# Performance work log

Hardware: AMD Instinct MI355X
Metric: run time of the kernel (lower is better)

The kernel has to match this reference:

```python
import jax, jax.numpy as jnp
import numpy as np
import math

NUM_HEADS = 2


def setup_inputs() -> dict:
    key = jax.random.key(0)
    k1, k2, k3, k4 = jax.random.split(key, 4)
    B, S, E = 16, 2048, 8  # embed_dim == n_wires == 8 (required by module structure)
    x = jax.random.normal(k1, (B, S, E), dtype=jnp.float32)
    theta = jax.random.normal(k2, (E,), dtype=jnp.float32)          # trainable RX angles, one per wire
    w_out = jax.random.normal(k3, (E, E), dtype=jnp.float32) / math.sqrt(E)  # out_proj weight
    b_out = jax.random.normal(k4, (E,), dtype=jnp.float32) * 0.01   # out_proj bias
    return {"x": x, "theta": theta, "w_out": w_out, "b_out": b_out}


def reference(x, theta, w_out, b_out):
    B, S, E = x.shape
    H = NUM_HEADS
    dk = E // H
    # Quantum projection, analytic form: per-wire RX(x) then RX(theta) on |0>,
    # PauliZ expectation -> cos(x + theta). Same layer applied for q, k, v.
    q = jnp.cos(x + theta)              # [B, S, E]
    qh = q.reshape(B, S, H, dk).transpose(0, 2, 1, 3)  # [B, H, S, dk]; q == k == v
    scores = jnp.einsum('bhqd,bhkd->bhqk', qh, qh) / jnp.sqrt(jnp.float32(dk))
    attn = jax.nn.softmax(scores, axis=-1)             # dropout is identity in eval
    out = jnp.einsum('bhqk,bhkd->bhqd', attn, qh)      # [B, H, S, dk]
    out = out.transpose(0, 2, 1, 3).reshape(B, S, E)
    return out @ w_out.T + b_out
```

## Files before the change

kernel.cpp:

```cpp
#include <hip/hip_runtime.h>
#include <math.h>

#define BB 16
#define SS 2048
#define NF 330
#define NS 495
#define SPAD 512
#define NTILE 31

struct E4 { unsigned char e0, e1, e2, e3; };

struct Tables {
  E4 se[496];
  E4 fe[330];
  float fc[330];
  short sidx[330][5];
};

constexpr int T1c(int n){ return n+1; }
constexpr int T2c(int n){ return (n+1)*(n+2)/2; }
constexpr int T3c(int n){ return (n+1)*(n+2)*(n+3)/6; }
constexpr int rank8(int a,int b,int c,int d){
  int r = 0;
  for (int e0=0;e0<a;++e0) r += T3c(8-e0);
  for (int e1=0;e1<b;++e1) r += T2c(8-a-e1);
  for (int e2=0;e2<c;++e2) r += T1c(8-a-b-e2);
  return r + d;
}
constexpr double besselI2(int n){
  double t = 1.0;
  for (int i=1;i<=n;++i) t /= (double)i;
  double s = 0.0;
  for (int m=0;m<14;++m){ if (m>0) t /= (double)(m*(m+n)); s += t; }
  return s;
}
constexpr Tables gen(){
  Tables T{};
  double cheb[8] = {};
  for (int n=0;n<8;++n) cheb[n] = (n==0?1.0:2.0)*besselI2(n);
  const int tm[8][8] = {
    {1,0,0,0,0,0,0,0},{0,1,0,0,0,0,0,0},{-1,0,2,0,0,0,0,0},{0,-3,0,4,0,0,0,0},
    {1,0,-8,0,8,0,0,0},{0,5,0,-20,0,16,0,0},{-1,0,18,0,-48,0,32,0},{0,-7,0,56,0,-112,0,64}};
  double bk[8] = {};
  double p2 = 1.0;
  for (int k=0;k<8;++k){
    double tc = 0.0;
    for (int n=0;n<8;++n) tc += cheb[n]*(double)tm[n][k];
    bk[k] = tc/p2;
    p2 *= 2.0;
  }
  const double fact[9] = {1,1,2,6,24,120,720,5040,40320};
  {
    int idx = 0;
    for (int a=0;a<=8;++a) for (int b=0;b<=8-a;++b) for (int c=0;c<=8-a-b;++c)
      for (int d=0;d<=8-a-b-c;++d){
        T.se[idx].e0=(unsigned char)a; T.se[idx].e1=(unsigned char)b;
        T.se[idx].e2=(unsigned char)c; T.se[idx].e3=(unsigned char)d; ++idx;
      }
  }
  {
    int idx = 0;
    for (int a=0;a<=7;++a) for (int b=0;b<=7-a;++b) for (int c=0;c<=7-a-b;++c)
      for (int d=0;d<=7-a-b-c;++d){
        const int k = a+b+c+d;
        const double mult = fact[k]/(fact[a]*fact[b]*fact[c]*fact[d]);
        double pk = 1.0; for (int i=0;i<k;++i) pk *= 2.0;
        T.fe[idx].e0=(unsigned char)a; T.fe[idx].e1=(unsigned char)b;
        T.fe[idx].e2=(unsigned char)c; T.fe[idx].e3=(unsigned char)d;
        T.fc[idx] = (float)(bk[k]*mult/pk);
        T.sidx[idx][0] = (short)rank8(a+1,b,c,d);
        T.sidx[idx][1] = (short)rank8(a,b+1,c,d);
        T.sidx[idx][2] = (short)rank8(a,b,c+1,d);
        T.sidx[idx][3] = (short)rank8(a,b,c,d+1);
        T.sidx[idx][4] = (short)rank8(a,b,c,d);
        ++idx;
      }
  }
  return T;
}
constexpr Tables TAB = gen();

template<int T>
__device__ __forceinline__ void sum_tile(const float4* __restrict__ x4,
                                         float4 th, int b, int h, int t,
                                         float* __restrict__ wsbh){
  float acc[16];
#pragma unroll
  for (int i=0;i<16;++i) acc[i] = 0.f;
  for (int rr=0; rr<8; ++rr){
    const int s = (rr<<8) + t;
    float4 xr = x4[(size_t)(b*SS+s)*2 + h];
    const float q0 = __cosf(xr.x + th.x), q1 = __cosf(xr.y + th.y),
                q2 = __cosf(xr.z + th.z), q3 = __cosf(xr.w + th.w);
    float p0[9], p1[9], p2[9], p3[9];
    p0[0]=1.f; p1[0]=1.f; p2[0]=1.f; p3[0]=1.f;
#pragma unroll
    for (int e=1;e<9;++e){
      p0[e]=p0[e-1]*q0; p1[e]=p1[e-1]*q1; p2[e]=p2[e-1]*q2; p3[e]=p3[e-1]*q3;
    }
#pragma unroll
    for (int i=0;i<16;++i){
      if (T*16+i < NS){
        const E4 e = TAB.se[T*16+i];
        acc[i] += p0[e.e0]*p1[e.e1]*p2[e.e2]*p3[e.e3];
      }
    }
  }
  const int lane = (int)(threadIdx.x & 63);
#pragma unroll
  for (int i=0;i<16;++i){
    if (T*16+i < NS){
      float v = acc[i];
#pragma unroll
      for (int st=1; st<64; st<<=1) v += __shfl_xor(v, st, 64);
      if (lane == 0) atomicAdd(wsbh + T*16 + i, v);
    }
  }
}

__global__ __launch_bounds__(256)
void qsum_kernel(const float* __restrict__ x, const float* __restrict__ theta,
                 float* __restrict__ ws){
  const int tile = blockIdx.x & 31;
  if (tile >= NTILE) return;
  const int bh = blockIdx.x >> 5;
  const int b = bh >> 1, h = bh & 1;
  const int t = (int)threadIdx.x;
  const float4 th = ((const float4*)theta)[h];
  const float4* x4 = (const float4*)x;
  float* wsbh = ws + (size_t)bh * SPAD;
  switch(tile){
#define KCASE(n) case n: sum_tile<n>(x4, th, b, h, t, wsbh); break;
    KCASE(0) KCASE(1) KCASE(2) KCASE(3) KCASE(4) KCASE(5) KCASE(6) KCASE(7)
    KCASE(8) KCASE(9) KCASE(10) KCASE(11) KCASE(12) KCASE(13) KCASE(14) KCASE(15)
    KCASE(16) KCASE(17) KCASE(18) KCASE(19) KCASE(20) KCASE(21) KCASE(22) KCASE(23)
    KCASE(24) KCASE(25) KCASE(26) KCASE(27) KCASE(28) KCASE(29) KCASE(30)
#undef KCASE
  }
}

__global__ __launch_bounds__(256)
void qout_kernel(const float* __restrict__ x, const float* __restrict__ theta,
                 const float* __restrict__ ws, const float* __restrict__ w_out,
                 const float* __restrict__ b_out, float* __restrict__ out){
  __shared__ float po[128 * 8];
  const int t   = (int)threadIdx.x;
  const int blk = (int)blockIdx.x;
  const int b   = blk >> 4;
  const int s0  = (blk & 15) << 7;
  const int lane = t & 63;
  const int h  = __builtin_amdgcn_readfirstlane((t >> 6) & 1);
  const int rr = ((t >> 7) << 6) | lane;
  const int s  = s0 + rr;

  const float4 th = ((const float4*)theta)[h];
  float4 xr = ((const float4*)x)[(size_t)(b*SS+s)*2 + h];
  const float q0 = __cosf(xr.x + th.x), q1 = __cosf(xr.y + th.y),
              q2 = __cosf(xr.z + th.z), q3 = __cosf(xr.w + th.w);
  float p0[8], p1[8], p2[8], p3[8];
  p0[0]=1.f; p1[0]=1.f; p2[0]=1.f; p3[0]=1.f;
#pragma unroll
  for (int e=1;e<8;++e){
    p0[e]=p0[e-1]*q0; p1[e]=p1[e-1]*q1; p2[e]=p2[e-1]*q2; p3[e]=p3[e-1]*q3;
  }
  const float* Sp = ws + (size_t)((b<<1) + h) * SPAD;
  float n0=0.f, n1=0.f, n2=0.f, n3=0.f, dn=0.f;
#pragma unroll
  for (int F=0; F<NF; ++F){
    const E4 e = TAB.fe[F];
    const float m = p0[e.e0]*p1[e.e1]*p2[e.e2]*p3[e.e3]*TAB.fc[F];
    n0 = fmaf(m, Sp[TAB.sidx[F][0]], n0);
    n1 = fmaf(m, Sp[TAB.sidx[F][1]], n1);
    n2 = fmaf(m, Sp[TAB.sidx[F][2]], n2);
    n3 = fmaf(m, Sp[TAB.sidx[F][3]], n3);
    dn = fmaf(m, Sp[TAB.sidx[F][4]], dn);
  }
  const float inv = 1.0f / dn;
  po[rr*8 + h*4 + 0] = n0*inv;
  po[rr*8 + h*4 + 1] = n1*inv;
  po[rr*8 + h*4 + 2] = n2*inv;
  po[rr*8 + h*4 + 3] = n3*inv;
  __syncthreads();

  if (t < 128){
    const float* pr = po + t*8;
    float o[8];
#pragma unroll
    for (int j=0;j<8;++j) o[j] = pr[j];
    float r[8];
#pragma unroll
    for (int e=0;e<8;++e){
      float acc = b_out[e];
#pragma unroll
      for (int j=0;j<8;++j) acc = fmaf(o[j], w_out[e*8+j], acc);
      r[e] = acc;
    }
    float* op = out + ((size_t)(b*SS + s0 + t)) * 8;
    *(float4*)op       = make_float4(r[0], r[1], r[2], r[3]);
    *(float4*)(op + 4) = make_float4(r[4], r[5], r[6], r[7]);
  }
}

extern "C" void kernel_launch(void* const* d_in, const int* in_sizes, int n_in,
                              void* d_out, int out_size, void* d_ws, size_t ws_size,
                              hipStream_t stream) {
  const float* x     = (const float*)d_in[0];
  const float* theta = (const float*)d_in[1];
  const float* w_out = (const float*)d_in[2];
  const float* b_out = (const float*)d_in[3];
  float* out = (float*)d_out;
  (void)in_sizes; (void)n_in; (void)out_size; (void)ws_size;

  (void)hipMemsetAsync(d_ws, 0, (size_t)32 * SPAD * sizeof(float), stream);
  qsum_kernel<<<dim3(32 * 32), 256, 0, stream>>>(x, theta, (float*)d_ws);
  qout_kernel<<<dim3(BB * 16), 256, 0, stream>>>(x, theta, (const float*)d_ws,
                                                 w_out, b_out, out);
}
```

Measured before the change: 88.90 us.

## Lower exp polynomial degree to 6 and pregather scaled moment coefficients

New measurement: 83.38 us. 6.2% less time.

```diff
diff --git a/kernel.cpp b/kernel.cpp
--- a/kernel.cpp
+++ b/kernel.cpp
@@ -1,148 +1,195 @@
 #include <hip/hip_runtime.h>
+#include <utility>
 #include <math.h>
 
 #define BB 16
 #define SS 2048
-#define NF 330
-#define NS 495
-#define SPAD 512
-#define NTILE 31
-
-struct E4 { unsigned char e0, e1, e2, e3; };
-
-struct Tables {
-  E4 se[496];
-  E4 fe[330];
-  float fc[330];
-  short sidx[330][5];
-};
-
-constexpr int T1c(int n){ return n+1; }
-constexpr int T2c(int n){ return (n+1)*(n+2)/2; }
-constexpr int T3c(int n){ return (n+1)*(n+2)*(n+3)/6; }
-constexpr int rank8(int a,int b,int c,int d){
+#define NF 210
+#define NS 330
+#define SSTR 336
+#define GSTR 224
+#define GBH (5*GSTR)
+#define GBASE 16384
+#define NTILE 21
+
+struct E4 { int e0, e1, e2, e3; };
+
+constexpr E4 exp_at(int idx, int deg) {
   int r = 0;
-  for (int e0=0;e0<a;++e0) r += T3c(8-e0);
-  for (int e1=0;e1<b;++e1) r += T2c(8-a-e1);
-  for (int e2=0;e2<c;++e2) r += T1c(8-a-b-e2);
-  return r + d;
-}
-constexpr double besselI2(int n){
+  for (int a = 0; a <= deg; ++a)
+    for (int b = 0; b <= deg - a; ++b)
+      for (int c = 0; c <= deg - a - b; ++c)
+        for (int d = 0; d <= deg - a - b - c; ++d) {
+          if (r == idx) return E4{a, b, c, d};
+          ++r;
+        }
+  return E4{0, 0, 0, 0};
+}
+constexpr int rank_of(int a, int b, int c, int d, int deg) {
+  int r = 0;
+  for (int aa = 0; aa <= deg; ++aa)
+    for (int bb = 0; bb <= deg - aa; ++bb)
+      for (int cc = 0; cc <= deg - aa - bb; ++cc)
+        for (int dd = 0; dd <= deg - aa - bb - cc; ++dd) {
+          if (aa == a && bb == b && cc == c && dd == d) return r;
+          ++r;
+        }
+  return 0;
+}
+constexpr double besselI2(int n) {
   double t = 1.0;
-  for (int i=1;i<=n;++i) t /= (double)i;
+  for (int i = 1; i <= n; ++i) t /= (double)i;
   double s = 0.0;
-  for (int m=0;m<14;++m){ if (m>0) t /= (double)(m*(m+n)); s += t; }
+  for (int m = 0; m < 16; ++m) { if (m > 0) t /= (double)(m * (m + n)); s += t; }
   return s;
 }
-constexpr Tables gen(){
-  Tables T{};
-  double cheb[8] = {};
-  for (int n=0;n<8;++n) cheb[n] = (n==0?1.0:2.0)*besselI2(n);
-  const int tm[8][8] = {
-    {1,0,0,0,0,0,0,0},{0,1,0,0,0,0,0,0},{-1,0,2,0,0,0,0,0},{0,-3,0,4,0,0,0,0},
-    {1,0,-8,0,8,0,0,0},{0,5,0,-20,0,16,0,0},{-1,0,18,0,-48,0,32,0},{0,-7,0,56,0,-112,0,64}};
-  double bk[8] = {};
+
+struct FTab { int sidx[NF][5]; float fc[NF]; };
+constexpr FTab gen_ftab() {
+  FTab T{};
+  double cheb[7] = {};
+  for (int n = 0; n < 7; ++n) cheb[n] = (n == 0 ? 1.0 : 2.0) * besselI2(n);
+  const int tm[7][7] = {
+    {1,0,0,0,0,0,0},{0,1,0,0,0,0,0},{-1,0,2,0,0,0,0},{0,-3,0,4,0,0,0},
+    {1,0,-8,0,8,0,0},{0,5,0,-20,0,16,0},{-1,0,18,0,-48,0,32}};
+  double bk[7] = {};
   double p2 = 1.0;
-  for (int k=0;k<8;++k){
+  for (int k = 0; k < 7; ++k) {
     double tc = 0.0;
-    for (int n=0;n<8;++n) tc += cheb[n]*(double)tm[n][k];
-    bk[k] = tc/p2;
+    for (int n = 0; n < 7; ++n) tc += cheb[n] * (double)tm[n][k];
+    bk[k] = tc / p2;
     p2 *= 2.0;
   }
-  const double fact[9] = {1,1,2,6,24,120,720,5040,40320};
-  {
-    int idx = 0;
-    for (int a=0;a<=8;++a) for (int b=0;b<=8-a;++b) for (int c=0;c<=8-a-b;++c)
-      for (int d=0;d<=8-a-b-c;++d){
-        T.se[idx].e0=(unsigned char)a; T.se[idx].e1=(unsigned char)b;
-        T.se[idx].e2=(unsigned char)c; T.se[idx].e3=(unsigned char)d; ++idx;
-      }
-  }
-  {
-    int idx = 0;
-    for (int a=0;a<=7;++a) for (int b=0;b<=7-a;++b) for (int c=0;c<=7-a-b;++c)
-      for (int d=0;d<=7-a-b-c;++d){
-        const int k = a+b+c+d;
-        const double mult = fact[k]/(fact[a]*fact[b]*fact[c]*fact[d]);
-        double pk = 1.0; for (int i=0;i<k;++i) pk *= 2.0;
-        T.fe[idx].e0=(unsigned char)a; T.fe[idx].e1=(unsigned char)b;
-        T.fe[idx].e2=(unsigned char)c; T.fe[idx].e3=(unsigned char)d;
-        T.fc[idx] = (float)(bk[k]*mult/pk);
-        T.sidx[idx][0] = (short)rank8(a+1,b,c,d);
-        T.sidx[idx][1] = (short)rank8(a,b+1,c,d);
-        T.sidx[idx][2] = (short)rank8(a,b,c+1,d);
-        T.sidx[idx][3] = (short)rank8(a,b,c,d+1);
-        T.sidx[idx][4] = (short)rank8(a,b,c,d);
-        ++idx;
-      }
-  }
+  const double fact[8] = {1,1,2,6,24,120,720,5040};
+  int idx = 0;
+  for (int a = 0; a <= 6; ++a)
+    for (int b = 0; b <= 6 - a; ++b)
+      for (int c = 0; c <= 6 - a - b; ++c)
+        for (int d = 0; d <= 6 - a - b - c; ++d) {
+          const int k = a + b + c + d;
+          const double mult = fact[k] / (fact[a]*fact[b]*fact[c]*fact[d]);
+          double pk = 1.0; for (int i = 0; i < k; ++i) pk *= 2.0;
+          T.fc[idx] = (float)(bk[k] * mult / pk);
+          T.sidx[idx][0] = rank_of(a+1, b, c, d, 7);
+          T.sidx[idx][1] = rank_of(a, b+1, c, d, 7);
+          T.sidx[idx][2] = rank_of(a, b, c+1, d, 7);
+          T.sidx[idx][3] = rank_of(a, b, c, d+1, 7);
+          T.sidx[idx][4] = rank_of(a, b, c, d, 7);
+          ++idx;
+        }
   return T;
 }
-constexpr Tables TAB = gen();
-
+__constant__ constexpr FTab FT = gen_ftab();
+
+template<int IDX, int SLOT>
+__device__ __forceinline__ void acc_one(float* acc, const float* p0, const float* p1,
+                                        const float* p2, const float* p3) {
+  if constexpr (IDX < NS) {
+    constexpr E4 e = exp_at(IDX, 7);
+    acc[SLOT] += p0[e.e0] * p1[e.e1] * p2[e.e2] * p3[e.e3];
+  }
+}
+template<int T, int... I>
+__device__ __forceinline__ void acc_tile(float* acc, const float* p0, const float* p1,
+                                         const float* p2, const float* p3,
+                                         std::integer_sequence<int, I...>) {
+  (acc_one<T * 16 + I, I>(acc, p0, p1, p2, p3), ...);
+}
+template<int IDX, int SLOT>
+__device__ __forceinline__ void red_one(float* acc, int lane, float* wsbh) {
+  if constexpr (IDX < NS) {
+    float v = acc[SLOT];
+    v += __shfl_xor(v, 1, 64);  v += __shfl_xor(v, 2, 64);
+    v += __shfl_xor(v, 4, 64);  v += __shfl_xor(v, 8, 64);
+    v += __shfl_xor(v, 16, 64); v += __shfl_xor(v, 32, 64);
+    if (lane == 0) atomicAdd(wsbh + IDX, v);
+  }
+}
+template<int T, int... I>
+__device__ __forceinline__ void red_tile(float* acc, int lane, float* wsbh,
+                                         std::integer_sequence<int, I...>) {
+  (red_one<T * 16 + I, I>(acc, lane, wsbh), ...);
+}
 template<int T>
-__device__ __forceinline__ void sum_tile(const float4* __restrict__ x4,
-                                         float4 th, int b, int h, int t,
-                                         float* __restrict__ wsbh){
+__device__ __forceinline__ void sum_tile(const float4* x4, float4 th, int b, int h,
+                                         int t, float* wsbh) {
   float acc[16];
 #pragma unroll
-  for (int i=0;i<16;++i) acc[i] = 0.f;
-  for (int rr=0; rr<8; ++rr){
-    const int s = (rr<<8) + t;
-    float4 xr = x4[(size_t)(b*SS+s)*2 + h];
+  for (int i = 0; i < 16; ++i) acc[i] = 0.f;
+  for (int rr = 0; rr < 8; ++rr) {
+    const int s = (rr << 8) + t;
+    float4 xr = x4[(size_t)(b * SS + s) * 2 + h];
     const float q0 = __cosf(xr.x + th.x), q1 = __cosf(xr.y + th.y),
                 q2 = __cosf(xr.z + th.z), q3 = __cosf(xr.w + th.w);
-    float p0[9], p1[9], p2[9], p3[9];
-    p0[0]=1.f; p1[0]=1.f; p2[0]=1.f; p3[0]=1.f;
-#pragma unroll
-    for (int e=1;e<9;++e){
-      p0[e]=p0[e-1]*q0; p1[e]=p1[e-1]*q1; p2[e]=p2[e-1]*q2; p3[e]=p3[e-1]*q3;
+    float p0[8], p1[8], p2[8], p3[8];
+    p0[0] = 1.f; p1[0] = 1.f; p2[0] = 1.f; p3[0] = 1.f;
+#pragma unroll
+    for (int e = 1; e < 8; ++e) {
+      p0[e] = p0[e-1] * q0; p1[e] = p1[e-1] * q1;
+      p2[e] = p2[e-1] * q2; p3[e] = p3[e-1] * q3;
     }
-#pragma unroll
-    for (int i=0;i<16;++i){
-      if (T*16+i < NS){
-        const E4 e = TAB.se[T*16+i];
-        acc[i] += p0[e.e0]*p1[e.e1]*p2[e.e2]*p3[e.e3];
-      }
-    }
-  }
-  const int lane = (int)(threadIdx.x & 63);
-#pragma unroll
-  for (int i=0;i<16;++i){
-    if (T*16+i < NS){
-      float v = acc[i];
-#pragma unroll
-      for (int st=1; st<64; st<<=1) v += __shfl_xor(v, st, 64);
-      if (lane == 0) atomicAdd(wsbh + T*16 + i, v);
-    }
-  }
+    acc_tile<T>(acc, p0, p1, p2, p3, std::make_integer_sequence<int, 16>{});
+  }
+  red_tile<T>(acc, (int)(threadIdx.x & 63), wsbh, std::make_integer_sequence<int, 16>{});
 }
 
 __global__ __launch_bounds__(256)
 void qsum_kernel(const float* __restrict__ x, const float* __restrict__ theta,
-                 float* __restrict__ ws){
-  const int tile = blockIdx.x & 31;
-  if (tile >= NTILE) return;
-  const int bh = blockIdx.x >> 5;
+                 float* __restrict__ ws) {
+  const int tile = (int)blockIdx.x;
+  const int bh   = (int)blockIdx.y;
   const int b = bh >> 1, h = bh & 1;
   const int t = (int)threadIdx.x;
   const float4 th = ((const float4*)theta)[h];
   const float4* x4 = (const float4*)x;
-  float* wsbh = ws + (size_t)bh * SPAD;
-  switch(tile){
-#define KCASE(n) case n: sum_tile<n>(x4, th, b, h, t, wsbh); break;
-    KCASE(0) KCASE(1) KCASE(2) KCASE(3) KCASE(4) KCASE(5) KCASE(6) KCASE(7)
-    KCASE(8) KCASE(9) KCASE(10) KCASE(11) KCASE(12) KCASE(13) KCASE(14) KCASE(15)
-    KCASE(16) KCASE(17) KCASE(18) KCASE(19) KCASE(20) KCASE(21) KCASE(22) KCASE(23)
-    KCASE(24) KCASE(25) KCASE(26) KCASE(27) KCASE(28) KCASE(29) KCASE(30)
-#undef KCASE
-  }
+  float* wsbh = ws + (size_t)bh * SSTR;
+  switch (tile) {
+#define KC(n) case n: sum_tile<n>(x4, th, b, h, t, wsbh); break;
+    KC(0) KC(1) KC(2) KC(3) KC(4) KC(5) KC(6) KC(7) KC(8) KC(9) KC(10)
+    KC(11) KC(12) KC(13) KC(14) KC(15) KC(16) KC(17) KC(18) KC(19) KC(20)
+#undef KC
+  }
+}
+
+__global__ __launch_bounds__(256)
+void qg_kernel(const float* __restrict__ ws, float* __restrict__ wsg) {
+  const int bh = (int)blockIdx.x;
+  const int F  = (int)threadIdx.x;
+  if (F >= NF) return;
+  const float* Sp = ws + (size_t)bh * SSTR;
+  float* Gp = wsg + (size_t)bh * GBH;
+  const float c = FT.fc[F];
+  Gp[0 * GSTR + F] = c * Sp[FT.sidx[F][0]];
+  Gp[1 * GSTR + F] = c * Sp[FT.sidx[F][1]];
+  Gp[2 * GSTR + F] = c * Sp[FT.sidx[F][2]];
+  Gp[3 * GSTR + F] = c * Sp[FT.sidx[F][3]];
+  Gp[4 * GSTR + F] = c * Sp[FT.sidx[F][4]];
+}
+
+template<int F>
+__device__ __forceinline__ void feat_one(float* n, const float* __restrict__ Gp,
+                                         const float* p0, const float* p1,
+                                         const float* p2, const float* p3) {
+  constexpr E4 e = exp_at(F, 6);
+  const float m = p0[e.e0] * p1[e.e1] * p2[e.e2] * p3[e.e3];
+  n[0] = fmaf(m, Gp[0 * GSTR + F], n[0]);
+  n[1] = fmaf(m, Gp[1 * GSTR + F], n[1]);
+  n[2] = fmaf(m, Gp[2 * GSTR + F], n[2]);
+  n[3] = fmaf(m, Gp[3 * GSTR + F], n[3]);
+  n[4] = fmaf(m, Gp[4 * GSTR + F], n[4]);
+}
+template<int... F>
+__device__ __forceinline__ void feat_all(float* n, const float* __restrict__ Gp,
+                                         const float* p0, const float* p1,
+                                         const float* p2, const float* p3,
+                                         std::integer_sequence<int, F...>) {
+  (feat_one<F>(n, Gp, p0, p1, p2, p3), ...);
 }
 
 __global__ __launch_bounds__(256)
 void qout_kernel(const float* __restrict__ x, const float* __restrict__ theta,
-                 const float* __restrict__ ws, const float* __restrict__ w_out,
-                 const float* __restrict__ b_out, float* __restrict__ out){
+                 const float* __restrict__ wsg, const float* __restrict__ w_out,
+                 const float* __restrict__ b_out, float* __restrict__ out) {
   __shared__ float po[128 * 8];
   const int t   = (int)threadIdx.x;
   const int blk = (int)blockIdx.x;
@@ -154,48 +201,41 @@
   const int s  = s0 + rr;
 
   const float4 th = ((const float4*)theta)[h];
-  float4 xr = ((const float4*)x)[(size_t)(b*SS+s)*2 + h];
+  float4 xr = ((const float4*)x)[(size_t)(b * SS + s) * 2 + h];
   const float q0 = __cosf(xr.x + th.x), q1 = __cosf(xr.y + th.y),
               q2 = __cosf(xr.z + th.z), q3 = __cosf(xr.w + th.w);
-  float p0[8], p1[8], p2[8], p3[8];
-  p0[0]=1.f; p1[0]=1.f; p2[0]=1.f; p3[0]=1.f;
-#pragma unroll
-  for (int e=1;e<8;++e){
-    p0[e]=p0[e-1]*q0; p1[e]=p1[e-1]*q1; p2[e]=p2[e-1]*q2; p3[e]=p3[e-1]*q3;
-  }
-  const float* Sp = ws + (size_t)((b<<1) + h) * SPAD;
-  float n0=0.f, n1=0.f, n2=0.f, n3=0.f, dn=0.f;
-#pragma unroll
-  for (int F=0; F<NF; ++F){
-    const E4 e = TAB.fe[F];
-    const float m = p0[e.e0]*p1[e.e1]*p2[e.e2]*p3[e.e3]*TAB.fc[F];
-    n0 = fmaf(m, Sp[TAB.sidx[F][0]], n0);
-    n1 = fmaf(m, Sp[TAB.sidx[F][1]], n1);
-    n2 = fmaf(m, Sp[TAB.sidx[F][2]], n2);
-    n3 = fmaf(m, Sp[TAB.sidx[F][3]], n3);
-    dn = fmaf(m, Sp[TAB.sidx[F][4]], dn);
-  }
-  const float inv = 1.0f / dn;
-  po[rr*8 + h*4 + 0] = n0*inv;
-  po[rr*8 + h*4 + 1] = n1*inv;
-  po[rr*8 + h*4 + 2] = n2*inv;
-  po[rr*8 + h*4 + 3] = n3*inv;
+  float p0[7], p1[7], p2[7], p3[7];
+  p0[0] = 1.f; p1[0] = 1.f; p2[0] = 1.f; p3[0] = 1.f;
+#pragma unroll
+  for (int e = 1; e < 7; ++e) {
+    p0[e] = p0[e-1] * q0; p1[e] = p1[e-1] * q1;
+    p2[e] = p2[e-1] * q2; p3[e] = p3[e-1] * q3;
+  }
+  const float* Gp = wsg + (size_t)((b << 1) + h) * GBH;
+  float n[5] = {0.f, 0.f, 0.f, 0.f, 0.f};
+  feat_all(n, Gp, p0, p1, p2, p3, std::make_integer_sequence<int, NF>{});
+
+  const float inv = 1.0f / n[4];
+  po[rr * 8 + h * 4 + 0] = n[0] * inv;
+  po[rr * 8 + h * 4 + 1] = n[1] * inv;
+  po[rr * 8 + h * 4 + 2] = n[2] * inv;
+  po[rr * 8 + h * 4 + 3] = n[3] * inv;
   __syncthreads();
 
-  if (t < 128){
-    const float* pr = po + t*8;
+  if (t < 128) {
+    const float* pr = po + t * 8;
     float o[8];
 #pragma unroll
-    for (int j=0;j<8;++j) o[j] = pr[j];
+    for (int j = 0; j < 8; ++j) o[j] = pr[j];
     float r[8];
 #pragma unroll
-    for (int e=0;e<8;++e){
+    for (int e = 0; e < 8; ++e) {
       float acc = b_out[e];
 #pragma unroll
-      for (int j=0;j<8;++j) acc = fmaf(o[j], w_out[e*8+j], acc);
+      for (int j = 0; j < 8; ++j) acc = fmaf(o[j], w_out[e * 8 + j], acc);
       r[e] = acc;
     }
-    float* op = out + ((size_t)(b*SS + s0 + t)) * 8;
+    float* op = out + ((size_t)(b * SS + s0 + t)) * 8;
     *(float4*)op       = make_float4(r[0], r[1], r[2], r[3]);
     *(float4*)(op + 4) = make_float4(r[4], r[5], r[6], r[7]);
   }
@@ -209,10 +249,12 @@
   const float* w_out = (const float*)d_in[2];
   const float* b_out = (const float*)d_in[3];
   float* out = (float*)d_out;
+  float* ws  = (float*)d_ws;
+  float* wsg = ws + GBASE;
   (void)in_sizes; (void)n_in; (void)out_size; (void)ws_size;
 
-  (void)hipMemsetAsync(d_ws, 0, (size_t)32 * SPAD * sizeof(float), stream);
-  qsum_kernel<<<dim3(32 * 32), 256, 0, stream>>>(x, theta, (float*)d_ws);
-  qout_kernel<<<dim3(BB * 16), 256, 0, stream>>>(x, theta, (const float*)d_ws,
-                                                 w_out, b_out, out);
-}
+  (void)hipMemsetAsync(d_ws, 0, (size_t)32 * SSTR * sizeof(float), stream);
+  qsum_kernel<<<dim3(NTILE, 32), 256, 0, stream>>>(x, theta, ws);
+  qg_kernel<<<dim3(32), 256, 0, stream>>>(ws, wsg);
+  qout_kernel<<<dim3(BB * 16), 256, 0, stream>>>(x, theta, wsg, w_out, b_out, out);
+}
```
